# Kernel tuning notes

Hardware: AMD Instinct MI355X
Metric: run time of the kernel (lower is better)

Reference implementation:

```python
import jax, jax.numpy as jnp
import numpy as np

RATIO = 0.7
N_NODES = 100000
N_EDGES = 800000
C = 128
HID = C // 2  # 64


def setup_inputs() -> dict:
    key = jax.random.key(0)
    k1, k2, k3, k4 = jax.random.split(key, 4)
    x = jax.random.normal(k1, (N_NODES, C), dtype=jnp.float32)
    edge_index = jax.random.randint(k2, (2, N_EDGES), 0, N_NODES, dtype=jnp.int64)
    # Glorot-ish scaled weights
    W1 = jax.random.normal(k3, (C, C + HID), dtype=jnp.float32) * (1.0 / np.sqrt(C))
    b1 = jnp.zeros((C + HID,), dtype=jnp.float32)
    W2 = jax.random.normal(k4, (C + HID, 1), dtype=jnp.float32) * (1.0 / np.sqrt(C + HID))
    b2 = jnp.zeros((1,), dtype=jnp.float32)
    return {"x": x, "edge_index": edge_index, "W1": W1, "b1": b1, "W2": W2, "b2": b2}


def reference(x, edge_index, W1, b1, W2, b2):
    n = x.shape[0]
    src = edge_index[0]
    dst = edge_index[1]
    ones = jnp.ones((edge_index.shape[1],), dtype=x.dtype)
    out_deg = jax.ops.segment_sum(ones, src, num_segments=n)
    in_deg = jax.ops.segment_sum(ones, dst, num_segments=n)
    # DGL GraphConv norm='both': clamp degree to >=1, symmetric normalization
    norm_src = jax.lax.rsqrt(jnp.maximum(out_deg, 1.0))  # [N]
    norm_dst = jax.lax.rsqrt(jnp.maximum(in_deg, 1.0))   # [N]

    def gconv(h, W, b):
        # h: [N, F_in] -> [N, F_out]
        msg = (h * norm_src[:, None])[src]                 # [E, F_in] gather
        agg = jax.ops.segment_sum(msg, dst, num_segments=n)  # [N, F_in] scatter-add
        return (agg * norm_dst[:, None]) @ W + b

    score = jax.nn.relu(gconv(x, W1, b1))                 # [N, C+HID]
    scores = gconv(score, W2, b2).squeeze(-1)             # [N]

    k = int(n * RATIO)
    _, idx = jax.lax.top_k(jnp.abs(scores), k)            # topk by |score|
    kept = jnp.sort(idx)  # remove_nodes keeps remaining nodes in original-id order
    return x[kept]                                        # [k, C]
```

## Files before the change

kernel.cpp:

```cpp
#include <hip/hip_runtime.h>
#include <stdint.h>

constexpr int C = 128;
constexpr int F1 = 192;

__global__ void k_detect(const int* __restrict__ ei, int E, int* __restrict__ res) {
    int t = blockIdx.x * 256 + threadIdx.x;
    int idx = 2 * t + 1;
    if (idx < 2 * E && ei[idx] != 0) atomicOr(&res[5], 1);
}

__global__ void k_deg(const int* __restrict__ ei, int E, const int* __restrict__ res,
                      int* __restrict__ outdeg, int* __restrict__ indeg) {
    int e = blockIdx.x * 256 + threadIdx.x;
    if (e < E) {
        bool i64 = (res[5] == 0);
        int s = i64 ? ei[2 * e]       : ei[e];
        int d = i64 ? ei[2 * (E + e)] : ei[E + e];
        atomicAdd(&outdeg[s], 1);
        atomicAdd(&indeg[d], 1);
    }
}

__global__ void scan1(const int* __restrict__ in, int* __restrict__ out,
                      int* __restrict__ bsums, int n,
                      const int* __restrict__ outdeg, float* __restrict__ nsrc,
                      float* __restrict__ ndst) {
    __shared__ int sh[1024];
    int i = blockIdx.x * 1024 + threadIdx.x;
    int v = (i < n) ? in[i] : 0;
    if (nsrc && i < n) {
        int od = outdeg[i]; if (od < 1) od = 1;
        int id = v;         if (id < 1) id = 1;
        nsrc[i] = (float)(1.0 / sqrt((double)od));
        ndst[i] = (float)(1.0 / sqrt((double)id));
    }
    sh[threadIdx.x] = v;
    __syncthreads();
    for (int off = 1; off < 1024; off <<= 1) {
        int t = (threadIdx.x >= off) ? sh[threadIdx.x - off] : 0;
        __syncthreads();
        sh[threadIdx.x] += t;
        __syncthreads();
    }
    if (i < n) out[i] = sh[threadIdx.x] - v;
    if (threadIdx.x == 1023) bsums[blockIdx.x] = sh[1023];
}

__global__ void scan2(int* __restrict__ bsums, int nb) {
    __shared__ int sh[1024];
    int t = threadIdx.x;
    int v = (t < nb) ? bsums[t] : 0;
    sh[t] = v;
    __syncthreads();
    for (int off = 1; off < 1024; off <<= 1) {
        int u = (t >= off) ? sh[t - off] : 0;
        __syncthreads();
        sh[t] += u;
        __syncthreads();
    }
    if (t < nb) bsums[t] = sh[t] - v;
}

__global__ void scan3(int* __restrict__ data, const int* __restrict__ bsums,
                      int* __restrict__ copy2, int n) {
    int i = blockIdx.x * 1024 + threadIdx.x;
    if (i < n) {
        int v = data[i] + bsums[blockIdx.x];
        data[i] = v;
        if (copy2) copy2[i] = v;
    }
}

__global__ void k_csr(const int* __restrict__ ei, int E, const int* __restrict__ res,
                      int* __restrict__ cursor, int* __restrict__ csr) {
    int e = blockIdx.x * 256 + threadIdx.x;
    if (e < E) {
        bool i64 = (res[5] == 0);
        int s = i64 ? ei[2 * e]       : ei[e];
        int d = i64 ? ei[2 * (E + e)] : ei[E + e];
        int p = atomicAdd(&cursor[d], 1);
        csr[p] = s;
    }
}

__global__ __launch_bounds__(256) void k_agg(const float* __restrict__ x,
        int* __restrict__ csr, const int* __restrict__ indeg,
        const int* __restrict__ offsets, const float* __restrict__ nsrc,
        const float* __restrict__ ndst, float* __restrict__ g, int N) {
    int wid  = (blockIdx.x * 256 + threadIdx.x) >> 6;
    int lane = threadIdx.x & 63;
    if (wid >= N) return;
    int deg = indeg[wid];
    int off = offsets[wid];
    float acc0 = 0.f, acc1 = 0.f;
    if (deg > 0 && deg <= 64) {
        int v = (lane < deg) ? csr[off + lane] : 0x7fffffff;
        int rank = 0;
        for (int j = 0; j < deg; ++j) {
            int vj = __builtin_amdgcn_readlane(v, j);
            rank += (vj < v) || (vj == v && j < lane);
        }
        int sv = __builtin_amdgcn_ds_permute(rank << 2, v);
        if (lane < deg) csr[off + lane] = sv;
        float nsv = (lane < deg) ? nsrc[sv] : 0.f;
        int nsb = __float_as_int(nsv);
        int i = 0;
        for (; i + 1 < deg; i += 2) {
            int   s0 = __builtin_amdgcn_readlane(sv, i);
            int   s1 = __builtin_amdgcn_readlane(sv, i + 1);
            float n0 = __int_as_float(__builtin_amdgcn_readlane(nsb, i));
            float n1 = __int_as_float(__builtin_amdgcn_readlane(nsb, i + 1));
            float2 x0 = ((const float2*)x)[(size_t)s0 * 64 + lane];
            float2 x1 = ((const float2*)x)[(size_t)s1 * 64 + lane];
            acc0 = fmaf(x0.x, n0, acc0);
            acc1 = fmaf(x0.y, n0, acc1);
            acc0 = fmaf(x1.x, n1, acc0);
            acc1 = fmaf(x1.y, n1, acc1);
        }
        if (i < deg) {
            int   s0 = __builtin_amdgcn_readlane(sv, i);
            float n0 = __int_as_float(__builtin_amdgcn_readlane(nsb, i));
            float2 x0 = ((const float2*)x)[(size_t)s0 * 64 + lane];
            acc0 = fmaf(x0.x, n0, acc0);
            acc1 = fmaf(x0.y, n0, acc1);
        }
    } else if (deg > 64) {
        for (int i = 0; i < deg; ++i) {
            int s = csr[off + i];
            float ns = nsrc[s];
            float2 xr = ((const float2*)x)[(size_t)s * 64 + lane];
            acc0 = fmaf(xr.x, ns, acc0);
            acc1 = fmaf(xr.y, ns, acc1);
        }
    }
    float nd = ndst[wid];
    ((float2*)g)[(size_t)wid * 64 + lane] = make_float2(acc0 * nd, acc1 * nd);
}

__global__ __launch_bounds__(256, 3) void k_gemm(const float* __restrict__ g,
        const float* __restrict__ W1, const float* __restrict__ b1,
        const float* __restrict__ W2, const float* __restrict__ nsrc,
        float* __restrict__ tn, int N) {
    __shared__ float At[32 * 132];
    __shared__ float Wt[32 * 200];
    int T  = threadIdx.x;
    int ng = T >> 4, jg = T & 15;
    int nb = blockIdx.x * 128;
    float acc[8][12];
    #pragma unroll
    for (int jj = 0; jj < 12; ++jj) {
        float b = b1[jg * 12 + jj];
        #pragma unroll
        for (int i = 0; i < 8; ++i) acc[i][jj] = b;
    }
    for (int s = 0; s < 4; ++s) {
        int k0 = s * 32;
        if (s) __syncthreads();
        int kq = T & 7;
        #pragma unroll
        for (int t = 0; t < 4; ++t) {
            int nl = (T >> 3) + 32 * t;
            int node = nb + nl;
            float4 v = make_float4(0.f, 0.f, 0.f, 0.f);
            if (node < N) v = *(const float4*)(g + (size_t)node * 128 + k0 + kq * 4);
            int base = (kq * 4) * 132 + nl;
            At[base]       = v.x;
            At[base + 132] = v.y;
            At[base + 264] = v.z;
            At[base + 396] = v.w;
        }
        #pragma unroll
        for (int i = 0; i < 6; ++i) {
            int idx = i * 256 + T;
            int r = idx / 48, j4 = idx - r * 48;
            float4 v = *(const float4*)(W1 + (k0 + r) * 192 + j4 * 4);
            *(float4*)&Wt[r * 200 + j4 * 4] = v;
        }
        __syncthreads();
        for (int kk = 0; kk < 32; ++kk) {
            float4 a0 = *(const float4*)&At[kk * 132 + ng * 8];
            float4 a1 = *(const float4*)&At[kk * 132 + ng * 8 + 4];
            float4 w0 = *(const float4*)&Wt[kk * 200 + jg * 12];
            float4 w1 = *(const float4*)&Wt[kk * 200 + jg * 12 + 4];
            float4 w2 = *(const float4*)&Wt[kk * 200 + jg * 12 + 8];
            float a[8]  = {a0.x, a0.y, a0.z, a0.w, a1.x, a1.y, a1.z, a1.w};
            float w[12] = {w0.x, w0.y, w0.z, w0.w, w1.x, w1.y, w1.z, w1.w,
                           w2.x, w2.y, w2.z, w2.w};
            #pragma unroll
            for (int i = 0; i < 8; ++i) {
                #pragma unroll
                for (int jj = 0; jj < 12; ++jj)
                    acc[i][jj] = fmaf(a[i], w[jj], acc[i][jj]);
            }
        }
    }
    float w2r[12];
    #pragma unroll
    for (int jj = 0; jj < 12; ++jj) w2r[jj] = W2[jg * 12 + jj];
    #pragma unroll
    for (int i = 0; i < 8; ++i) {
        float p = 0.f;
        #pragma unroll
        for (int jj = 0; jj < 12; ++jj) p = fmaf(fmaxf(acc[i][jj], 0.f), w2r[jj], p);
        p += __shfl_xor(p, 1);
        p += __shfl_xor(p, 2);
        p += __shfl_xor(p, 4);
        p += __shfl_xor(p, 8);
        if (jg == 0) {
            int node = nb + ng * 8 + i;
            if (node < N) tn[node] = p * nsrc[node];
        }
    }
}

__global__ void k_l2(const int* __restrict__ csr, const int* __restrict__ indeg,
                     const int* __restrict__ offsets, const float* __restrict__ tn,
                     const float* __restrict__ ndst, const float* __restrict__ b2,
                     unsigned int* __restrict__ U, int* __restrict__ hist1, int N) {
    int n = blockIdx.x * 256 + threadIdx.x;
    if (n >= N) return;
    int deg = indeg[n], off = offsets[n];
    float s = 0.f;
    for (int i = 0; i < deg; ++i) s += tn[csr[off + i]];
    float sc = ndst[n] * s + b2[0];
    unsigned int u = __float_as_uint(fabsf(sc));
    U[n] = u;
    atomicAdd(&hist1[u >> 16], 1);
}

__global__ void k_findbin1(const int* __restrict__ hist, int k, int* __restrict__ res) {
    __shared__ int sh[1024];
    int t = threadIdx.x;
    int base = 65535 - 64 * t;
    int s = 0;
    for (int q = 0; q < 64; ++q) s += hist[base - q];
    sh[t] = s;
    __syncthreads();
    int v = s;
    for (int off = 1; off < 1024; off <<= 1) {
        int u = (t >= off) ? sh[t - off] : 0;
        __syncthreads();
        sh[t] += u;
        __syncthreads();
    }
    int before = sh[t] - v;
    if (before < k && sh[t] >= k) {
        int cum = before;
        for (int q = 0; q < 64; ++q) {
            int b = base - q;
            int hh = hist[b];
            if (cum + hh >= k) { res[0] = b; res[1] = k - cum; break; }
            cum += hh;
        }
    }
}

__global__ void k_hist2(const unsigned int* __restrict__ U, const int* __restrict__ res,
                        int* __restrict__ hist2, int N) {
    int n = blockIdx.x * 256 + threadIdx.x;
    if (n < N) {
        unsigned int u = U[n];
        if ((int)(u >> 16) == res[0]) atomicAdd(&hist2[u & 0xffff], 1);
    }
}

__global__ void k_findbin2(const int* __restrict__ hist, int* __restrict__ res) {
    __shared__ int sh[1024];
    int k = res[1];
    int t = threadIdx.x;
    int base = 65535 - 64 * t;
    int s = 0;
    for (int q = 0; q < 64; ++q) s += hist[base - q];
    sh[t] = s;
    __syncthreads();
    int v = s;
    for (int off = 1; off < 1024; off <<= 1) {
        int u = (t >= off) ? sh[t - off] : 0;
        __syncthreads();
        sh[t] += u;
        __syncthreads();
    }
    int before = sh[t] - v;
    if (before < k && sh[t] >= k) {
        int cum = before;
        for (int q = 0; q < 64; ++q) {
            int b = base - q;
            int hh = hist[b];
            if (cum + hh >= k) {
                res[2] = (int)(((unsigned int)res[0] << 16) | (unsigned int)b);
                res[3] = k - cum;
                break;
            }
            cum += hh;
        }
    }
}

__global__ void k_flags(const unsigned int* __restrict__ U, int* __restrict__ res,
                        int* __restrict__ sel, int* __restrict__ tielist, int N) {
    int n = blockIdx.x * 256 + threadIdx.x;
    if (n >= N) return;
    unsigned int T = (unsigned int)res[2];
    unsigned int u = U[n];
    sel[n] = (u > T) ? 1 : 0;
    if (u == T) {
        int p = atomicAdd(&res[4], 1);
        if (p < 4096) tielist[p] = n;
    }
}

__global__ void k_ties(const int* __restrict__ res, int* __restrict__ tielist,
                       int* __restrict__ sel) {
    if (threadIdx.x != 0) return;
    int cnt = res[4]; if (cnt > 4096) cnt = 4096;
    int need = res[3]; if (need > cnt) need = cnt;
    for (int r = 0; r < need; ++r) {
        int mi = 0, mv = 0x7fffffff;
        for (int i = 0; i < cnt; ++i) {
            int v = tielist[i];
            if (v < mv) { mv = v; mi = i; }
        }
        sel[mv] = 1;
        tielist[mi] = 0x7fffffff;
    }
}

__global__ __launch_bounds__(256) void k_out(const float* __restrict__ x,
        const int* __restrict__ sel, const int* __restrict__ pos,
        float* __restrict__ out, int N) {
    int wid  = (blockIdx.x * 256 + threadIdx.x) >> 6;
    int lane = threadIdx.x & 63;
    if (wid >= N) return;
    if (sel[wid]) {
        int p = pos[wid];
        ((float2*)out)[(size_t)p * 64 + lane] = ((const float2*)x)[(size_t)wid * 64 + lane];
    }
}

extern "C" void kernel_launch(void* const* d_in, const int* in_sizes, int n_in,
                              void* d_out, int out_size, void* d_ws, size_t ws_size,
                              hipStream_t stream) {
    const float* x  = (const float*)d_in[0];
    const int*   ei = (const int*)d_in[1];
    const float* W1 = (const float*)d_in[2];
    const float* b1 = (const float*)d_in[3];
    const float* W2 = (const float*)d_in[4];
    const float* b2 = (const float*)d_in[5];
    int N = in_sizes[0] / C;
    int E = in_sizes[1] / 2;
    int k = out_size / C;

    char* w = (char*)d_ws;
    size_t ofs = 0;
    auto alloc = [&](size_t bytes) -> char* {
        char* p = w + ofs;
        ofs += (bytes + 511) & ~(size_t)511;
        return p;
    };
    int*   outdeg  = (int*)alloc((size_t)N * 4);
    int*   indeg   = (int*)alloc((size_t)N * 4);
    int*   hist1   = (int*)alloc(65536 * 4);
    int*   hist2   = (int*)alloc(65536 * 4);
    int*   res     = (int*)alloc(64);
    size_t zero_bytes = ofs;
    int*   offsets = (int*)alloc((size_t)(N + 1) * 4);
    int*   cursor  = (int*)alloc((size_t)N * 4);
    int*   csr     = (int*)alloc((size_t)E * 4);
    float* nsrc    = (float*)alloc((size_t)N * 4);
    float* ndst    = (float*)alloc((size_t)N * 4);
    float* g       = (float*)alloc((size_t)N * C * 4);
    float* tn      = (float*)alloc((size_t)N * 4);
    unsigned int* U = (unsigned int*)alloc((size_t)N * 4);
    int*   tielist = (int*)alloc(4096 * 4);
    int*   sel     = (int*)alloc((size_t)N * 4);
    int*   pos     = (int*)alloc((size_t)N * 4);
    int*   bsums   = (int*)alloc(1024 * 4);

    hipMemsetAsync(d_ws, 0, zero_bytes, stream);

    int nb = (N + 1023) / 1024;
    k_detect<<<16, 256, 0, stream>>>(ei, E, res);
    k_deg<<<(E + 255) / 256, 256, 0, stream>>>(ei, E, res, outdeg, indeg);
    scan1<<<nb, 1024, 0, stream>>>(indeg, offsets, bsums, N, outdeg, nsrc, ndst);
    scan2<<<1, 1024, 0, stream>>>(bsums, nb);
    scan3<<<nb, 1024, 0, stream>>>(offsets, bsums, cursor, N);
    k_csr<<<(E + 255) / 256, 256, 0, stream>>>(ei, E, res, cursor, csr);
    k_agg<<<(N + 3) / 4, 256, 0, stream>>>(x, csr, indeg, offsets, nsrc, ndst, g, N);
    k_gemm<<<(N + 127) / 128, 256, 0, stream>>>(g, W1, b1, W2, nsrc, tn, N);
    k_l2<<<(N + 255) / 256, 256, 0, stream>>>(csr, indeg, offsets, tn, ndst, b2, U, hist1, N);
    k_findbin1<<<1, 1024, 0, stream>>>(hist1, k, res);
    k_hist2<<<(N + 255) / 256, 256, 0, stream>>>(U, res, hist2, N);
    k_findbin2<<<1, 1024, 0, stream>>>(hist2, res);
    k_flags<<<(N + 255) / 256, 256, 0, stream>>>(U, res, sel, tielist, N);
    k_ties<<<1, 64, 0, stream>>>(res, tielist, sel);
    scan1<<<nb, 1024, 0, stream>>>(sel, pos, bsums, N, nullptr, nullptr, nullptr);
    scan2<<<1, 1024, 0, stream>>>(bsums, nb);
    scan3<<<nb, 1024, 0, stream>>>(pos, bsums, nullptr, N);
    k_out<<<(N + 3) / 4, 256, 0, stream>>>(x, sel, pos, (float*)d_out, N);
}
```

Measured before the change: 481.0 us.

## Fuse scan passes, replace serial tie kernel with packed prefix scan, enlarge GEMM tile

```diff
diff --git a/kernel.cpp b/kernel.cpp
--- a/kernel.cpp
+++ b/kernel.cpp
@@ -47,26 +47,20 @@
     if (threadIdx.x == 1023) bsums[blockIdx.x] = sh[1023];
 }
 
-__global__ void scan2(int* __restrict__ bsums, int nb) {
+__global__ void scan3b(int* __restrict__ data, const int* __restrict__ bsums,
+                       int* __restrict__ copy2, int n) {
     __shared__ int sh[1024];
     int t = threadIdx.x;
-    int v = (t < nb) ? bsums[t] : 0;
-    sh[t] = v;
-    __syncthreads();
-    for (int off = 1; off < 1024; off <<= 1) {
-        int u = (t >= off) ? sh[t - off] : 0;
-        __syncthreads();
-        sh[t] += u;
-        __syncthreads();
-    }
-    if (t < nb) bsums[t] = sh[t] - v;
-}
-
-__global__ void scan3(int* __restrict__ data, const int* __restrict__ bsums,
-                      int* __restrict__ copy2, int n) {
-    int i = blockIdx.x * 1024 + threadIdx.x;
+    sh[t] = (t < (int)blockIdx.x) ? bsums[t] : 0;
+    __syncthreads();
+    for (int off = 512; off > 0; off >>= 1) {
+        if (t < off) sh[t] += sh[t + off];
+        __syncthreads();
+    }
+    int boff = sh[0];
+    int i = blockIdx.x * 1024 + t;
     if (i < n) {
-        int v = data[i] + bsums[blockIdx.x];
+        int v = data[i] + boff;
         data[i] = v;
         if (copy2) copy2[i] = v;
     }
@@ -106,24 +100,29 @@
         float nsv = (lane < deg) ? nsrc[sv] : 0.f;
         int nsb = __float_as_int(nsv);
         int i = 0;
-        for (; i + 1 < deg; i += 2) {
+        for (; i + 3 < deg; i += 4) {
             int   s0 = __builtin_amdgcn_readlane(sv, i);
             int   s1 = __builtin_amdgcn_readlane(sv, i + 1);
+            int   s2 = __builtin_amdgcn_readlane(sv, i + 2);
+            int   s3 = __builtin_amdgcn_readlane(sv, i + 3);
             float n0 = __int_as_float(__builtin_amdgcn_readlane(nsb, i));
             float n1 = __int_as_float(__builtin_amdgcn_readlane(nsb, i + 1));
+            float n2 = __int_as_float(__builtin_amdgcn_readlane(nsb, i + 2));
+            float n3 = __int_as_float(__builtin_amdgcn_readlane(nsb, i + 3));
             float2 x0 = ((const float2*)x)[(size_t)s0 * 64 + lane];
             float2 x1 = ((const float2*)x)[(size_t)s1 * 64 + lane];
-            acc0 = fmaf(x0.x, n0, acc0);
-            acc1 = fmaf(x0.y, n0, acc1);
-            acc0 = fmaf(x1.x, n1, acc0);
-            acc1 = fmaf(x1.y, n1, acc1);
-        }
-        if (i < deg) {
+            float2 x2 = ((const float2*)x)[(size_t)s2 * 64 + lane];
+            float2 x3 = ((const float2*)x)[(size_t)s3 * 64 + lane];
+            acc0 = fmaf(x0.x, n0, acc0); acc1 = fmaf(x0.y, n0, acc1);
+            acc0 = fmaf(x1.x, n1, acc0); acc1 = fmaf(x1.y, n1, acc1);
+            acc0 = fmaf(x2.x, n2, acc0); acc1 = fmaf(x2.y, n2, acc1);
+            acc0 = fmaf(x3.x, n3, acc0); acc1 = fmaf(x3.y, n3, acc1);
+        }
+        for (; i < deg; ++i) {
             int   s0 = __builtin_amdgcn_readlane(sv, i);
             float n0 = __int_as_float(__builtin_amdgcn_readlane(nsb, i));
             float2 x0 = ((const float2*)x)[(size_t)s0 * 64 + lane];
-            acc0 = fmaf(x0.x, n0, acc0);
-            acc1 = fmaf(x0.y, n0, acc1);
+            acc0 = fmaf(x0.x, n0, acc0); acc1 = fmaf(x0.y, n0, acc1);
         }
     } else if (deg > 64) {
         for (int i = 0; i < deg; ++i) {
@@ -138,37 +137,37 @@
     ((float2*)g)[(size_t)wid * 64 + lane] = make_float2(acc0 * nd, acc1 * nd);
 }
 
-__global__ __launch_bounds__(256, 3) void k_gemm(const float* __restrict__ g,
+__global__ __launch_bounds__(256, 2) void k_gemm(const float* __restrict__ g,
         const float* __restrict__ W1, const float* __restrict__ b1,
         const float* __restrict__ W2, const float* __restrict__ nsrc,
         float* __restrict__ tn, int N) {
-    __shared__ float At[32 * 132];
+    __shared__ float At[32 * 196];
     __shared__ float Wt[32 * 200];
     int T  = threadIdx.x;
     int ng = T >> 4, jg = T & 15;
-    int nb = blockIdx.x * 128;
-    float acc[8][12];
+    int nb = blockIdx.x * 192;
+    float acc[12][12];
     #pragma unroll
     for (int jj = 0; jj < 12; ++jj) {
         float b = b1[jg * 12 + jj];
         #pragma unroll
-        for (int i = 0; i < 8; ++i) acc[i][jj] = b;
+        for (int i = 0; i < 12; ++i) acc[i][jj] = b;
     }
     for (int s = 0; s < 4; ++s) {
         int k0 = s * 32;
         if (s) __syncthreads();
         int kq = T & 7;
         #pragma unroll
-        for (int t = 0; t < 4; ++t) {
+        for (int t = 0; t < 6; ++t) {
             int nl = (T >> 3) + 32 * t;
             int node = nb + nl;
             float4 v = make_float4(0.f, 0.f, 0.f, 0.f);
             if (node < N) v = *(const float4*)(g + (size_t)node * 128 + k0 + kq * 4);
-            int base = (kq * 4) * 132 + nl;
+            int base = (kq * 4) * 196 + nl;
             At[base]       = v.x;
-            At[base + 132] = v.y;
-            At[base + 264] = v.z;
-            At[base + 396] = v.w;
+            At[base + 196] = v.y;
+            At[base + 392] = v.z;
+            At[base + 588] = v.w;
         }
         #pragma unroll
         for (int i = 0; i < 6; ++i) {
@@ -179,16 +178,18 @@
         }
         __syncthreads();
         for (int kk = 0; kk < 32; ++kk) {
-            float4 a0 = *(const float4*)&At[kk * 132 + ng * 8];
-            float4 a1 = *(const float4*)&At[kk * 132 + ng * 8 + 4];
+            float4 a0 = *(const float4*)&At[kk * 196 + ng * 12];
+            float4 a1 = *(const float4*)&At[kk * 196 + ng * 12 + 4];
+            float4 a2 = *(const float4*)&At[kk * 196 + ng * 12 + 8];
             float4 w0 = *(const float4*)&Wt[kk * 200 + jg * 12];
             float4 w1 = *(const float4*)&Wt[kk * 200 + jg * 12 + 4];
             float4 w2 = *(const float4*)&Wt[kk * 200 + jg * 12 + 8];
-            float a[8]  = {a0.x, a0.y, a0.z, a0.w, a1.x, a1.y, a1.z, a1.w};
+            float a[12] = {a0.x, a0.y, a0.z, a0.w, a1.x, a1.y, a1.z, a1.w,
+                           a2.x, a2.y, a2.z, a2.w};
             float w[12] = {w0.x, w0.y, w0.z, w0.w, w1.x, w1.y, w1.z, w1.w,
                            w2.x, w2.y, w2.z, w2.w};
             #pragma unroll
-            for (int i = 0; i < 8; ++i) {
+            for (int i = 0; i < 12; ++i) {
                 #pragma unroll
                 for (int jj = 0; jj < 12; ++jj)
                     acc[i][jj] = fmaf(a[i], w[jj], acc[i][jj]);
@@ -199,7 +200,7 @@
     #pragma unroll
     for (int jj = 0; jj < 12; ++jj) w2r[jj] = W2[jg * 12 + jj];
     #pragma unroll
-    for (int i = 0; i < 8; ++i) {
+    for (int i = 0; i < 12; ++i) {
         float p = 0.f;
         #pragma unroll
         for (int jj = 0; jj < 12; ++jj) p = fmaf(fmaxf(acc[i][jj], 0.f), w2r[jj], p);
@@ -208,7 +209,7 @@
         p += __shfl_xor(p, 4);
         p += __shfl_xor(p, 8);
         if (jg == 0) {
-            int node = nb + ng * 8 + i;
+            int node = nb + ng * 12 + i;
             if (node < N) tn[node] = p * nsrc[node];
         }
     }
@@ -297,32 +298,52 @@
     }
 }
 
-__global__ void k_flags(const unsigned int* __restrict__ U, int* __restrict__ res,
-                        int* __restrict__ sel, int* __restrict__ tielist, int N) {
-    int n = blockIdx.x * 256 + threadIdx.x;
-    if (n >= N) return;
+__global__ void pscan1(const unsigned int* __restrict__ U, const int* __restrict__ res,
+                       int* __restrict__ ppos, int* __restrict__ pbsums, int n) {
+    __shared__ int sh[1024];
     unsigned int T = (unsigned int)res[2];
-    unsigned int u = U[n];
-    sel[n] = (u > T) ? 1 : 0;
-    if (u == T) {
-        int p = atomicAdd(&res[4], 1);
-        if (p < 4096) tielist[p] = n;
-    }
-}
-
-__global__ void k_ties(const int* __restrict__ res, int* __restrict__ tielist,
-                       int* __restrict__ sel) {
-    if (threadIdx.x != 0) return;
-    int cnt = res[4]; if (cnt > 4096) cnt = 4096;
-    int need = res[3]; if (need > cnt) need = cnt;
-    for (int r = 0; r < need; ++r) {
-        int mi = 0, mv = 0x7fffffff;
-        for (int i = 0; i < cnt; ++i) {
-            int v = tielist[i];
-            if (v < mv) { mv = v; mi = i; }
-        }
-        sel[mv] = 1;
-        tielist[mi] = 0x7fffffff;
+    int i = blockIdx.x * 1024 + threadIdx.x;
+    int v = 0;
+    if (i < n) {
+        unsigned int u = U[i];
+        v = (u > T) ? 1 : ((u == T) ? 0x10000 : 0);
+    }
+    sh[threadIdx.x] = v;
+    __syncthreads();
+    for (int off = 1; off < 1024; off <<= 1) {
+        int t = (threadIdx.x >= off) ? sh[threadIdx.x - off] : 0;
+        __syncthreads();
+        sh[threadIdx.x] += t;
+        __syncthreads();
+    }
+    if (i < n) ppos[i] = sh[threadIdx.x] - v;
+    if (threadIdx.x == 1023) pbsums[blockIdx.x] = sh[1023];
+}
+
+__global__ void pscan2out(const unsigned int* __restrict__ U, const int* __restrict__ res,
+                          const int* __restrict__ ppos, const int* __restrict__ pbsums,
+                          int* __restrict__ sel, int* __restrict__ pos, int n) {
+    __shared__ int sg[1024], se[1024];
+    int t = threadIdx.x;
+    int b = (t < (int)blockIdx.x) ? pbsums[t] : 0;
+    sg[t] = b & 0xffff;
+    se[t] = b >> 16;
+    __syncthreads();
+    for (int off = 512; off > 0; off >>= 1) {
+        if (t < off) { sg[t] += sg[t + off]; se[t] += se[t + off]; }
+        __syncthreads();
+    }
+    int i = blockIdx.x * 1024 + t;
+    if (i < n) {
+        unsigned int T = (unsigned int)res[2];
+        int need = res[3];
+        unsigned int u = U[i];
+        int p = ppos[i];
+        int Pgt = (p & 0xffff) + sg[0];
+        int Peq = (p >> 16) + se[0];
+        int gt = (u > T), eq = (u == T);
+        sel[i] = gt | (eq & (Peq < need ? 1 : 0));
+        pos[i] = Pgt + (Peq < need ? Peq : need);
     }
 }
 
@@ -372,10 +393,10 @@
     float* g       = (float*)alloc((size_t)N * C * 4);
     float* tn      = (float*)alloc((size_t)N * 4);
     unsigned int* U = (unsigned int*)alloc((size_t)N * 4);
-    int*   tielist = (int*)alloc(4096 * 4);
     int*   sel     = (int*)alloc((size_t)N * 4);
     int*   pos     = (int*)alloc((size_t)N * 4);
     int*   bsums   = (int*)alloc(1024 * 4);
+    int*   pbsums  = (int*)alloc(1024 * 4);
 
     hipMemsetAsync(d_ws, 0, zero_bytes, stream);
 
@@ -383,19 +404,15 @@
     k_detect<<<16, 256, 0, stream>>>(ei, E, res);
     k_deg<<<(E + 255) / 256, 256, 0, stream>>>(ei, E, res, outdeg, indeg);
     scan1<<<nb, 1024, 0, stream>>>(indeg, offsets, bsums, N, outdeg, nsrc, ndst);
-    scan2<<<1, 1024, 0, stream>>>(bsums, nb);
-    scan3<<<nb, 1024, 0, stream>>>(offsets, bsums, cursor, N);
+    scan3b<<<nb, 1024, 0, stream>>>(offsets, bsums, cursor, N);
     k_csr<<<(E + 255) / 256, 256, 0, stream>>>(ei, E, res, cursor, csr);
     k_agg<<<(N + 3) / 4, 256, 0, stream>>>(x, csr, indeg, offsets, nsrc, ndst, g, N);
-    k_gemm<<<(N + 127) / 128, 256, 0, stream>>>(g, W1, b1, W2, nsrc, tn, N);
+    k_gemm<<<(N + 191) / 192, 256, 0, stream>>>(g, W1, b1, W2, nsrc, tn, N);
     k_l2<<<(N + 255) / 256, 256, 0, stream>>>(csr, indeg, offsets, tn, ndst, b2, U, hist1, N);
     k_findbin1<<<1, 1024, 0, stream>>>(hist1, k, res);
     k_hist2<<<(N + 255) / 256, 256, 0, stream>>>(U, res, hist2, N);
     k_findbin2<<<1, 1024, 0, stream>>>(hist2, res);
-    k_flags<<<(N + 255) / 256, 256, 0, stream>>>(U, res, sel, tielist, N);
-    k_ties<<<1, 64, 0, stream>>>(res, tielist, sel);
-    scan1<<<nb, 1024, 0, stream>>>(sel, pos, bsums, N, nullptr, nullptr, nullptr);
-    scan2<<<1, 1024, 0, stream>>>(bsums, nb);
-    scan3<<<nb, 1024, 0, stream>>>(pos, bsums, nullptr, N);
+    pscan1<<<nb, 1024, 0, stream>>>(U, res, pos, pbsums, N);
+    pscan2out<<<nb, 1024, 0, stream>>>(U, res, pos, pbsums, sel, pos, N);
     k_out<<<(N + 3) / 4, 256, 0, stream>>>(x, sel, pos, (float*)d_out, N);
 }
```

Result: no change. 490.5 us (+2.0%).

## Replace shared-memory scans with wave scans and fuse tie-selection into compaction

Applied to the files above, without the earlier changes.

```diff
diff --git a/kernel.cpp b/kernel.cpp
--- a/kernel.cpp
+++ b/kernel.cpp
@@ -3,6 +3,43 @@
 
 constexpr int C = 128;
 constexpr int F1 = 192;
+
+__device__ __forceinline__ int block_scan_incl(int v, int* sh16) {
+    int lane = threadIdx.x & 63;
+    int wv   = threadIdx.x >> 6;
+    int s = v;
+    #pragma unroll
+    for (int off = 1; off < 64; off <<= 1) {
+        int t = __shfl_up(s, off);
+        if (lane >= off) s += t;
+    }
+    if (lane == 63) sh16[wv] = s;
+    __syncthreads();
+    if (wv == 0) {
+        int w = (lane < 16) ? sh16[lane] : 0;
+        #pragma unroll
+        for (int off = 1; off < 16; off <<= 1) {
+            int t = __shfl_up(w, off);
+            if (lane >= off) w += t;
+        }
+        if (lane < 16) sh16[lane] = w;
+    }
+    __syncthreads();
+    return s + (wv ? sh16[wv - 1] : 0);
+}
+
+__device__ __forceinline__ int block_reduce_add(int v, int* sh16) {
+    #pragma unroll
+    for (int off = 32; off > 0; off >>= 1) v += __shfl_xor(v, off);
+    int lane = threadIdx.x & 63;
+    int wv   = threadIdx.x >> 6;
+    if (lane == 0) sh16[wv] = v;
+    __syncthreads();
+    int r = sh16[0];
+    #pragma unroll
+    for (int i = 1; i < 16; ++i) r += sh16[i];
+    return r;
+}
 
 __global__ void k_detect(const int* __restrict__ ei, int E, int* __restrict__ res) {
     int t = blockIdx.x * 256 + threadIdx.x;
@@ -26,7 +63,7 @@
                       int* __restrict__ bsums, int n,
                       const int* __restrict__ outdeg, float* __restrict__ nsrc,
                       float* __restrict__ ndst) {
-    __shared__ int sh[1024];
+    __shared__ int sh16[16];
     int i = blockIdx.x * 1024 + threadIdx.x;
     int v = (i < n) ? in[i] : 0;
     if (nsrc && i < n) {
@@ -35,40 +72,22 @@
         nsrc[i] = (float)(1.0 / sqrt((double)od));
         ndst[i] = (float)(1.0 / sqrt((double)id));
     }
-    sh[threadIdx.x] = v;
-    __syncthreads();
-    for (int off = 1; off < 1024; off <<= 1) {
-        int t = (threadIdx.x >= off) ? sh[threadIdx.x - off] : 0;
-        __syncthreads();
-        sh[threadIdx.x] += t;
-        __syncthreads();
-    }
-    if (i < n) out[i] = sh[threadIdx.x] - v;
-    if (threadIdx.x == 1023) bsums[blockIdx.x] = sh[1023];
-}
-
-__global__ void scan2(int* __restrict__ bsums, int nb) {
-    __shared__ int sh[1024];
+    int incl = block_scan_incl(v, sh16);
+    if (i < n) out[i] = incl - v;
+    if (threadIdx.x == 1023) bsums[blockIdx.x] = incl;
+}
+
+__global__ void scan3b(int* __restrict__ data, const int* __restrict__ bsums,
+                       int* __restrict__ copy2, int n) {
+    __shared__ int sh16[16];
     int t = threadIdx.x;
-    int v = (t < nb) ? bsums[t] : 0;
-    sh[t] = v;
-    __syncthreads();
-    for (int off = 1; off < 1024; off <<= 1) {
-        int u = (t >= off) ? sh[t - off] : 0;
-        __syncthreads();
-        sh[t] += u;
-        __syncthreads();
-    }
-    if (t < nb) bsums[t] = sh[t] - v;
-}
-
-__global__ void scan3(int* __restrict__ data, const int* __restrict__ bsums,
-                      int* __restrict__ copy2, int n) {
-    int i = blockIdx.x * 1024 + threadIdx.x;
+    int v = (t < (int)blockIdx.x) ? bsums[t] : 0;
+    int boff = block_reduce_add(v, sh16);
+    int i = blockIdx.x * 1024 + t;
     if (i < n) {
-        int v = data[i] + bsums[blockIdx.x];
-        data[i] = v;
-        if (copy2) copy2[i] = v;
+        int u = data[i] + boff;
+        data[i] = u;
+        if (copy2) copy2[i] = u;
     }
 }
 
@@ -106,24 +125,39 @@
         float nsv = (lane < deg) ? nsrc[sv] : 0.f;
         int nsb = __float_as_int(nsv);
         int i = 0;
-        for (; i + 1 < deg; i += 2) {
-            int   s0 = __builtin_amdgcn_readlane(sv, i);
-            int   s1 = __builtin_amdgcn_readlane(sv, i + 1);
-            float n0 = __int_as_float(__builtin_amdgcn_readlane(nsb, i));
-            float n1 = __int_as_float(__builtin_amdgcn_readlane(nsb, i + 1));
-            float2 x0 = ((const float2*)x)[(size_t)s0 * 64 + lane];
-            float2 x1 = ((const float2*)x)[(size_t)s1 * 64 + lane];
-            acc0 = fmaf(x0.x, n0, acc0);
-            acc1 = fmaf(x0.y, n0, acc1);
-            acc0 = fmaf(x1.x, n1, acc0);
-            acc1 = fmaf(x1.y, n1, acc1);
-        }
-        if (i < deg) {
+        for (; i + 7 < deg; i += 8) {
+            float2 xr[8]; float nn[8];
+            #pragma unroll
+            for (int q = 0; q < 8; ++q) {
+                int   sq = __builtin_amdgcn_readlane(sv, i + q);
+                nn[q]    = __int_as_float(__builtin_amdgcn_readlane(nsb, i + q));
+                xr[q] = ((const float2*)x)[(size_t)sq * 64 + lane];
+            }
+            #pragma unroll
+            for (int q = 0; q < 8; ++q) {
+                acc0 = fmaf(xr[q].x, nn[q], acc0);
+                acc1 = fmaf(xr[q].y, nn[q], acc1);
+            }
+        }
+        for (; i + 3 < deg; i += 4) {
+            float2 xr[4]; float nn[4];
+            #pragma unroll
+            for (int q = 0; q < 4; ++q) {
+                int   sq = __builtin_amdgcn_readlane(sv, i + q);
+                nn[q]    = __int_as_float(__builtin_amdgcn_readlane(nsb, i + q));
+                xr[q] = ((const float2*)x)[(size_t)sq * 64 + lane];
+            }
+            #pragma unroll
+            for (int q = 0; q < 4; ++q) {
+                acc0 = fmaf(xr[q].x, nn[q], acc0);
+                acc1 = fmaf(xr[q].y, nn[q], acc1);
+            }
+        }
+        for (; i < deg; ++i) {
             int   s0 = __builtin_amdgcn_readlane(sv, i);
             float n0 = __int_as_float(__builtin_amdgcn_readlane(nsb, i));
             float2 x0 = ((const float2*)x)[(size_t)s0 * 64 + lane];
-            acc0 = fmaf(x0.x, n0, acc0);
-            acc1 = fmaf(x0.y, n0, acc1);
+            acc0 = fmaf(x0.x, n0, acc0); acc1 = fmaf(x0.y, n0, acc1);
         }
     } else if (deg > 64) {
         for (int i = 0; i < deg; ++i) {
@@ -230,22 +264,19 @@
 }
 
 __global__ void k_findbin1(const int* __restrict__ hist, int k, int* __restrict__ res) {
-    __shared__ int sh[1024];
+    __shared__ int sh16[16];
     int t = threadIdx.x;
     int base = 65535 - 64 * t;
     int s = 0;
-    for (int q = 0; q < 64; ++q) s += hist[base - q];
-    sh[t] = s;
-    __syncthreads();
-    int v = s;
-    for (int off = 1; off < 1024; off <<= 1) {
-        int u = (t >= off) ? sh[t - off] : 0;
-        __syncthreads();
-        sh[t] += u;
-        __syncthreads();
-    }
-    int before = sh[t] - v;
-    if (before < k && sh[t] >= k) {
+    const int4* hv = (const int4*)(hist + base - 63);
+    #pragma unroll
+    for (int q = 0; q < 16; ++q) {
+        int4 h4 = hv[q];
+        s += h4.x + h4.y + h4.z + h4.w;
+    }
+    int incl = block_scan_incl(s, sh16);
+    int before = incl - s;
+    if (before < k && incl >= k) {
         int cum = before;
         for (int q = 0; q < 64; ++q) {
             int b = base - q;
@@ -266,23 +297,20 @@
 }
 
 __global__ void k_findbin2(const int* __restrict__ hist, int* __restrict__ res) {
-    __shared__ int sh[1024];
+    __shared__ int sh16[16];
     int k = res[1];
     int t = threadIdx.x;
     int base = 65535 - 64 * t;
     int s = 0;
-    for (int q = 0; q < 64; ++q) s += hist[base - q];
-    sh[t] = s;
-    __syncthreads();
-    int v = s;
-    for (int off = 1; off < 1024; off <<= 1) {
-        int u = (t >= off) ? sh[t - off] : 0;
-        __syncthreads();
-        sh[t] += u;
-        __syncthreads();
-    }
-    int before = sh[t] - v;
-    if (before < k && sh[t] >= k) {
+    const int4* hv = (const int4*)(hist + base - 63);
+    #pragma unroll
+    for (int q = 0; q < 16; ++q) {
+        int4 h4 = hv[q];
+        s += h4.x + h4.y + h4.z + h4.w;
+    }
+    int incl = block_scan_incl(s, sh16);
+    int before = incl - s;
+    if (before < k && incl >= k) {
         int cum = before;
         for (int q = 0; q < 64; ++q) {
             int b = base - q;
@@ -297,44 +325,60 @@
     }
 }
 
-__global__ void k_flags(const unsigned int* __restrict__ U, int* __restrict__ res,
-                        int* __restrict__ sel, int* __restrict__ tielist, int N) {
-    int n = blockIdx.x * 256 + threadIdx.x;
-    if (n >= N) return;
+__global__ void pscan1(const unsigned int* __restrict__ U, const int* __restrict__ res,
+                       int* __restrict__ ppos, int* __restrict__ pbsums, int n) {
+    __shared__ int sh16[16];
     unsigned int T = (unsigned int)res[2];
-    unsigned int u = U[n];
-    sel[n] = (u > T) ? 1 : 0;
-    if (u == T) {
-        int p = atomicAdd(&res[4], 1);
-        if (p < 4096) tielist[p] = n;
-    }
-}
-
-__global__ void k_ties(const int* __restrict__ res, int* __restrict__ tielist,
-                       int* __restrict__ sel) {
-    if (threadIdx.x != 0) return;
-    int cnt = res[4]; if (cnt > 4096) cnt = 4096;
-    int need = res[3]; if (need > cnt) need = cnt;
-    for (int r = 0; r < need; ++r) {
-        int mi = 0, mv = 0x7fffffff;
-        for (int i = 0; i < cnt; ++i) {
-            int v = tielist[i];
-            if (v < mv) { mv = v; mi = i; }
-        }
-        sel[mv] = 1;
-        tielist[mi] = 0x7fffffff;
-    }
-}
-
-__global__ __launch_bounds__(256) void k_out(const float* __restrict__ x,
-        const int* __restrict__ sel, const int* __restrict__ pos,
-        float* __restrict__ out, int N) {
-    int wid  = (blockIdx.x * 256 + threadIdx.x) >> 6;
-    int lane = threadIdx.x & 63;
-    if (wid >= N) return;
-    if (sel[wid]) {
-        int p = pos[wid];
-        ((float2*)out)[(size_t)p * 64 + lane] = ((const float2*)x)[(size_t)wid * 64 + lane];
+    int i = blockIdx.x * 1024 + threadIdx.x;
+    int v = 0;
+    if (i < n) {
+        unsigned int u = U[i];
+        v = (u > T) ? 1 : ((u == T) ? 0x10000 : 0);
+    }
+    int incl = block_scan_incl(v, sh16);
+    if (i < n) ppos[i] = incl - v;
+    if (threadIdx.x == 1023) pbsums[blockIdx.x] = incl;
+}
+
+__global__ void pscan2out(const unsigned int* __restrict__ U, const int* __restrict__ res,
+                          const int* __restrict__ ppos, const int* __restrict__ pbsums,
+                          const float* __restrict__ x, float* __restrict__ out, int n) {
+    __shared__ int shg[16], she[16];
+    int t = threadIdx.x;
+    int b = (t < (int)blockIdx.x) ? pbsums[t] : 0;
+    int gsum = b & 0xffff, esum = b >> 16;
+    #pragma unroll
+    for (int off = 32; off > 0; off >>= 1) {
+        gsum += __shfl_xor(gsum, off);
+        esum += __shfl_xor(esum, off);
+    }
+    int lane = t & 63, wv = t >> 6;
+    if (lane == 0) { shg[wv] = gsum; she[wv] = esum; }
+    __syncthreads();
+    int Gp = 0, Ep = 0;
+    #pragma unroll
+    for (int i = 0; i < 16; ++i) { Gp += shg[i]; Ep += she[i]; }
+    int i = blockIdx.x * 1024 + t;
+    int selbit = 0, posv = 0;
+    if (i < n) {
+        unsigned int T = (unsigned int)res[2];
+        int need = res[3];
+        unsigned int u = U[i];
+        int p = ppos[i];
+        int Pgt = (p & 0xffff) + Gp;
+        int Peq = (p >> 16) + Ep;
+        int gt = (u > T), eq = (u == T);
+        selbit = gt | (eq & (Peq < need ? 1 : 0));
+        posv = Pgt + (Peq < need ? Peq : need);
+    }
+    unsigned long long m = __ballot(selbit);
+    int nbase = blockIdx.x * 1024 + wv * 64;
+    while (m) {
+        int bit = __ffsll((long long)m) - 1;
+        m &= m - 1;
+        int p = __builtin_amdgcn_readlane(posv, bit);
+        int node = nbase + bit;
+        ((float2*)out)[(size_t)p * 64 + lane] = ((const float2*)x)[(size_t)node * 64 + lane];
     }
 }
 
@@ -372,10 +416,9 @@
     float* g       = (float*)alloc((size_t)N * C * 4);
     float* tn      = (float*)alloc((size_t)N * 4);
     unsigned int* U = (unsigned int*)alloc((size_t)N * 4);
-    int*   tielist = (int*)alloc(4096 * 4);
-    int*   sel     = (int*)alloc((size_t)N * 4);
-    int*   pos     = (int*)alloc((size_t)N * 4);
+    int*   ppos    = (int*)alloc((size_t)N * 4);
     int*   bsums   = (int*)alloc(1024 * 4);
+    int*   pbsums  = (int*)alloc(1024 * 4);
 
     hipMemsetAsync(d_ws, 0, zero_bytes, stream);
 
@@ -383,8 +426,7 @@
     k_detect<<<16, 256, 0, stream>>>(ei, E, res);
     k_deg<<<(E + 255) / 256, 256, 0, stream>>>(ei, E, res, outdeg, indeg);
     scan1<<<nb, 1024, 0, stream>>>(indeg, offsets, bsums, N, outdeg, nsrc, ndst);
-    scan2<<<1, 1024, 0, stream>>>(bsums, nb);
-    scan3<<<nb, 1024, 0, stream>>>(offsets, bsums, cursor, N);
+    scan3b<<<nb, 1024, 0, stream>>>(offsets, bsums, cursor, N);
     k_csr<<<(E + 255) / 256, 256, 0, stream>>>(ei, E, res, cursor, csr);
     k_agg<<<(N + 3) / 4, 256, 0, stream>>>(x, csr, indeg, offsets, nsrc, ndst, g, N);
     k_gemm<<<(N + 127) / 128, 256, 0, stream>>>(g, W1, b1, W2, nsrc, tn, N);
@@ -392,10 +434,6 @@
     k_findbin1<<<1, 1024, 0, stream>>>(hist1, k, res);
     k_hist2<<<(N + 255) / 256, 256, 0, stream>>>(U, res, hist2, N);
     k_findbin2<<<1, 1024, 0, stream>>>(hist2, res);
-    k_flags<<<(N + 255) / 256, 256, 0, stream>>>(U, res, sel, tielist, N);
-    k_ties<<<1, 64, 0, stream>>>(res, tielist, sel);
-    scan1<<<nb, 1024, 0, stream>>>(sel, pos, bsums, N, nullptr, nullptr, nullptr);
-    scan2<<<1, 1024, 0, stream>>>(bsums, nb);
-    scan3<<<nb, 1024, 0, stream>>>(pos, bsums, nullptr, N);
-    k_out<<<(N + 3) / 4, 256, 0, stream>>>(x, sel, pos, (float*)d_out, N);
-}
+    pscan1<<<nb, 1024, 0, stream>>>(U, res, ppos, pbsums, N);
+    pscan2out<<<nb, 1024, 0, stream>>>(U, res, ppos, pbsums, x, (float*)d_out, N);
+}
```

Result: faster. 468.8 us (-2.6%).
